# Kernel optimization log

Measured on AMD Instinct MI355X. Metric: run time of the kernel, lower is better.

## Reference

```python
import jax, jax.numpy as jnp
import numpy as np

B, H, TQ, TK, DH = 4, 8, 128, 128, 64
N_MEM, D_MEM, TOPK, HID = 100000, 512, 32, 128


def setup_inputs() -> dict:
    key = jax.random.key(0)
    ks = jax.random.split(key, 12)
    return {
        "q": jax.random.normal(ks[0], (B, H, TQ, DH), jnp.float32),
        "k_ctx": jax.random.normal(ks[1], (B, H, TK, DH), jnp.float32),
        "v_ctx": jax.random.normal(ks[2], (B, H, TK, DH), jnp.float32),
        "q_for_mem": jax.random.normal(ks[3], (B, TQ, D_MEM), jnp.float32),
        "mem_keys": jax.random.normal(ks[4], (N_MEM, D_MEM), jnp.float32),
        "mem_values": jax.random.normal(ks[5], (N_MEM, D_MEM), jnp.float32),
        "Wk": jax.random.normal(ks[6], (DH, D_MEM), jnp.float32) / np.sqrt(D_MEM),
        "Wv": jax.random.normal(ks[7], (DH, D_MEM), jnp.float32) / np.sqrt(D_MEM),
        "W1": jax.random.normal(ks[8], (HID, 2 * DH), jnp.float32) / np.sqrt(2 * DH),
        "b1": jnp.zeros((HID,), jnp.float32),
        "w2": jax.random.normal(ks[9], (HID,), jnp.float32) / np.sqrt(HID),
        "b2": jnp.zeros((1,), jnp.float32),
    }


def reference(q, k_ctx, v_ctx, q_for_mem, mem_keys, mem_values, Wk, Wv, W1, b1, w2, b2):
    # --- MemoryBank.retrieve: dense scores + top-k gather ---
    mem_scores = jnp.einsum('btd,nd->btn', q_for_mem, mem_keys)          # [B,TQ,N]
    _, idx = jax.lax.top_k(mem_scores, TOPK)                             # [B,TQ,K]
    K_mem = mem_keys[idx] @ Wk.T                                         # [B,TQ,K,DH] (mem_k_proj)
    V_mem = mem_values[idx] @ Wv.T                                       # [B,TQ,K,DH] (mem_v_proj)

    # --- ParametricScoreMLP: f([q;k]) = w2 . relu(W1q q + W1k k + b1) + b2 ---
    W1q, W1k = W1[:, :DH], W1[:, DH:]                                    # split concat linear
    q_part = jnp.einsum('bhtd,ed->bhte', q, W1q)                         # [B,H,TQ,HID]
    kctx_part = jnp.einsum('bhsd,ed->bhse', k_ctx, W1k)                  # [B,H,TK,HID]
    kmem_part = jnp.einsum('btkd,ed->btke', K_mem, W1k)                  # [B,TQ,K,HID]

    h_ctx = jax.nn.relu(q_part[:, :, :, None, :] + kctx_part[:, :, None, :, :] + b1)
    s_ctx = jnp.einsum('bhtse,e->bhts', h_ctx, w2) + b2[0]               # [B,H,TQ,TK]
    h_mem = jax.nn.relu(q_part[:, :, :, None, :] + kmem_part[:, None, :, :, :] + b1)
    s_mem = jnp.einsum('bhtke,e->bhtk', h_mem, w2) + b2[0]               # [B,H,TQ,K]

    scores = jnp.concatenate([s_ctx, s_mem], axis=-1)                    # [B,H,TQ,TK+K]
    weights = jax.nn.softmax(scores, axis=-1)

    w_ctx, w_mem = weights[..., :TK], weights[..., TK:]
    out = jnp.einsum('bhts,bhsd->bhtd', w_ctx, v_ctx) \
        + jnp.einsum('bhtk,btkd->bhtd', w_mem, V_mem)                    # [B,H,TQ,DH]
    return out, weights
```

## Files before the change

### kernel.cpp

```cpp
#include <hip/hip_runtime.h>
#include <cmath>

constexpr int B_ = 4, H_ = 8, TQ_ = 128, TK_ = 128, DH_ = 64;
constexpr int NMEM = 100000, DM = 512, TOPK = 32, HID = 128;
constexpr int R_ = B_ * TQ_;
constexpr int CTILE = 128, RTILE = 64;
constexpr int NCHP = 784;
constexpr int NPAD = NCHP * CTILE;
constexpr int KC = 16;
constexpr int NCAND = NCHP * KC;
constexpr int KSEL = 48;
constexpr int CAP  = 128;
constexpr int NLD  = NCAND / 256;

using f32x4  = __attribute__((ext_vector_type(4))) float;
using bf16x8 = __attribute__((ext_vector_type(8))) short;
using u16x8  = __attribute__((ext_vector_type(8))) unsigned short;

#define GLOAD16(g, l) __builtin_amdgcn_global_load_lds( \
    (const __attribute__((address_space(1))) void*)(g), \
    (__attribute__((address_space(3))) void*)(l), 16, 0, 0)

static __device__ __forceinline__ unsigned short f2bf(float f) {
    unsigned u = __float_as_uint(f);
    u = (u + 0x7FFFu + ((u >> 16) & 1u)) >> 16;
    return (unsigned short)u;
}

__global__ __launch_bounds__(256)
void k0_cvt(const float* __restrict__ src, unsigned short* __restrict__ dst,
            long n, long ntot)
{
    long stride = (long)gridDim.x * 256 * 8;
    for (long base = ((long)blockIdx.x * 256 + threadIdx.x) * 8; base < ntot; base += stride) {
        u16x8 o;
        if (base < n) {
            float4 v0 = *reinterpret_cast<const float4*>(src + base);
            float4 v1 = *reinterpret_cast<const float4*>(src + base + 4);
            o[0] = f2bf(v0.x); o[1] = f2bf(v0.y); o[2] = f2bf(v0.z); o[3] = f2bf(v0.w);
            o[4] = f2bf(v1.x); o[5] = f2bf(v1.y); o[6] = f2bf(v1.z); o[7] = f2bf(v1.w);
        } else {
            o = (u16x8)0;
        }
        *reinterpret_cast<u16x8*>(dst + base) = o;
    }
}

__global__ __launch_bounds__(256)
void k1_mfma(const unsigned short* __restrict__ qmb, const unsigned short* __restrict__ mkb,
             unsigned* __restrict__ cand_k, int* __restrict__ cand_i)
{
    const int wgid = blockIdx.x;
    const int xcd = wgid & 7;
    const int k9 = wgid >> 3;
    const int chunk = xcd * 98 + (k9 >> 3);
    const int rt = k9 & 7;
    const int row0 = rt * RTILE;
    const int col0 = chunk * CTILE;
    const int tid = threadIdx.x;
    const int lane = tid & 63, w = tid >> 6;
    const int wm = w >> 1, wn = w & 1;

    __shared__ __align__(16) char smem[64 * 132 * 4];
    char* Abase = smem;
    char* Bbase = smem + 8192;
    float* scf = (float*)smem;

    const char* srcA[2];
    const char* srcB[4];
#pragma unroll
    for (int p = 0; p < 2; ++p) {
        int X = p * 4096 + w * 1024 + lane * 16;
        int r = X >> 7, c = (X & 127) ^ ((r & 7) << 4);
        srcA[p] = (const char*)qmb + (size_t)(row0 + r) * 1024 + c;
    }
#pragma unroll
    for (int p = 0; p < 4; ++p) {
        int X = p * 4096 + w * 1024 + lane * 16;
        int r = X >> 7, c = (X & 127) ^ ((r & 7) << 4);
        srcB[p] = (const char*)mkb + (size_t)(col0 + r) * 1024 + c;
    }
    int aoff[2][2], boff[4][2];
#pragma unroll
    for (int mi = 0; mi < 2; ++mi) {
        int rr = wm * 32 + mi * 16 + (lane & 15);
        int bse = rr * 128 + ((lane >> 4) * 16);
        aoff[mi][0] = bse ^ ((rr & 7) << 4);
        aoff[mi][1] = (bse + 64) ^ ((rr & 7) << 4);
    }
#pragma unroll
    for (int ni = 0; ni < 4; ++ni) {
        int rr = wn * 64 + ni * 16 + (lane & 15);
        int bse = rr * 128 + ((lane >> 4) * 16);
        boff[ni][0] = 8192 + (bse ^ ((rr & 7) << 4));
        boff[ni][1] = 8192 + ((bse + 64) ^ ((rr & 7) << 4));
    }

    f32x4 acc[2][4];
#pragma unroll
    for (int mi = 0; mi < 2; ++mi)
#pragma unroll
        for (int ni = 0; ni < 4; ++ni) acc[mi][ni] = (f32x4)0.f;

    for (int ks = 0; ks < 8; ++ks) {
#pragma unroll
        for (int p = 0; p < 2; ++p) {
            GLOAD16(srcA[p], Abase + p * 4096 + w * 1024);
            srcA[p] += 128;
        }
#pragma unroll
        for (int p = 0; p < 4; ++p) {
            GLOAD16(srcB[p], Bbase + p * 4096 + w * 1024);
            srcB[p] += 128;
        }
        __syncthreads();
#pragma unroll
        for (int kk = 0; kk < 2; ++kk) {
            bf16x8 af[2], bfr[4];
#pragma unroll
            for (int mi = 0; mi < 2; ++mi)
                af[mi] = *reinterpret_cast<const bf16x8*>(smem + aoff[mi][kk]);
#pragma unroll
            for (int ni = 0; ni < 4; ++ni)
                bfr[ni] = *reinterpret_cast<const bf16x8*>(smem + boff[ni][kk]);
#pragma unroll
            for (int mi = 0; mi < 2; ++mi)
#pragma unroll
                for (int ni = 0; ni < 4; ++ni)
                    acc[mi][ni] = __builtin_amdgcn_mfma_f32_16x16x32_bf16(af[mi], bfr[ni], acc[mi][ni], 0, 0, 0);
        }
        __syncthreads();
    }

#pragma unroll
    for (int mi = 0; mi < 2; ++mi)
#pragma unroll
        for (int ni = 0; ni < 4; ++ni)
#pragma unroll
            for (int reg = 0; reg < 4; ++reg) {
                int rr = wm * 32 + mi * 16 + (lane >> 4) * 4 + reg;
                int cc = wn * 64 + ni * 16 + (lane & 15);
                scf[rr * 132 + cc] = (col0 + cc < NMEM) ? acc[mi][ni][reg] : -INFINITY;
            }
    __syncthreads();

    const int rid = tid >> 2, sub = tid & 3;
    const float* srow = scf + rid * 132;
    unsigned long long t0 = 0ull, t1 = 0ull, t2 = 0ull, t3 = 0ull;
#pragma unroll 8
    for (int i = 0; i < 32; ++i) {
        int c = sub + 4 * i;
        float v = srow[c];
        unsigned b = __float_as_uint(v);
        unsigned s = b ^ ((unsigned)((int)b >> 31) | 0x80000000u);
        unsigned long long k = ((unsigned long long)s << 7) | (unsigned)(127 - c);
        bool g0 = k > t0, g1 = k > t1, g2 = k > t2, g3 = k > t3;
        unsigned long long n0 = g0 ? k : t0;
        unsigned long long n1 = g0 ? t0 : (g1 ? k : t1);
        unsigned long long n2 = g1 ? t1 : (g2 ? k : t2);
        unsigned long long n3 = g2 ? t2 : (g3 ? k : t3);
        t0 = n0; t1 = n1; t2 = n2; t3 = n3;
    }
    size_t base = (size_t)(row0 + rid) * NCAND + (size_t)chunk * KC + sub * 4;
    uint4 kv, iv;
    kv.x = (unsigned)(t0 >> 7); iv.x = col0 + 127 - (int)(t0 & 127u);
    kv.y = (unsigned)(t1 >> 7); iv.y = col0 + 127 - (int)(t1 & 127u);
    kv.z = (unsigned)(t2 >> 7); iv.z = col0 + 127 - (int)(t2 & 127u);
    kv.w = (unsigned)(t3 >> 7); iv.w = col0 + 127 - (int)(t3 & 127u);
    *reinterpret_cast<uint4*>(cand_k + base) = kv;
    *reinterpret_cast<uint4*>(cand_i + base) = iv;
}

__global__ __launch_bounds__(256)
void k2a_thresh(const unsigned* __restrict__ cand_k, const int* __restrict__ cand_i,
                int* __restrict__ cand2_i, int* __restrict__ cand2_n)
{
    const int row = blockIdx.x;
    const int tid = threadIdx.x;
    const int lane = tid & 63, wv = tid >> 6;
    const unsigned* ck = cand_k + (size_t)row * NCAND;

    unsigned key[NLD];
#pragma unroll
    for (int j = 0; j < NLD; ++j) key[j] = ck[tid + j * 256];

    __shared__ int red[4];
    __shared__ int cnt;
    unsigned lo = 0u;
    int c_cur = NCAND;
    for (int bit = 31; bit >= 0; --bit) {
        if (c_cur <= CAP) break;
        unsigned T = lo | (1u << bit);
        int c = 0;
#pragma unroll
        for (int j = 0; j < NLD; ++j) c += (key[j] >= T);
#pragma unroll
        for (int off = 1; off < 64; off <<= 1) c += __shfl_xor(c, off);
        if (lane == 0) red[wv] = c;
        __syncthreads();
        int ct = red[0] + red[1] + red[2] + red[3];
        if (ct >= KSEL) { lo = T; c_cur = ct; }
        __syncthreads();
    }

    if (tid == 0) cnt = 0;
    __syncthreads();
#pragma unroll
    for (int j = 0; j < NLD; ++j) {
        if (key[j] >= lo) {
            int p = atomicAdd(&cnt, 1);
            if (p < CAP) cand2_i[(size_t)row * CAP + p] = cand_i[(size_t)row * NCAND + tid + j * 256];
        }
    }
    __syncthreads();
    if (tid == 0) cand2_n[row] = cnt < CAP ? cnt : CAP;
}

__global__ __launch_bounds__(256)
void k2b_rescore(const float* __restrict__ qm, const float* __restrict__ mk,
                 const int* __restrict__ cand2_i, const int* __restrict__ cand2_n,
                 double* __restrict__ rsc)
{
    const int row = blockIdx.x;
    const int tid = threadIdx.x;
    const int lane = tid & 63, wv = tid >> 6;
    const int c = blockIdx.y * 4 + wv;
    const int n = cand2_n[row];
    if (c >= n) return;
    const int idx = cand2_i[(size_t)row * CAP + c];
    const float* qrow = qm + (size_t)row * DM;
    const float* krow = mk + (size_t)idx * DM;
    double p = 0.0;
#pragma unroll
    for (int j = 0; j < DM / 64; ++j) {
        int d = lane + j * 64;
        p += (double)qrow[d] * (double)krow[d];
    }
#pragma unroll
    for (int off = 1; off < 64; off <<= 1) p += __shfl_xor(p, off);
    if (lane == 0) rsc[(size_t)row * CAP + c] = p;
}

__global__ __launch_bounds__(64)
void k2c_top32(const double* __restrict__ rsc, const int* __restrict__ cand2_i,
               const int* __restrict__ cand2_n, int* __restrict__ sel)
{
    const int row = blockIdx.x;
    const int lane = threadIdx.x;
    const int n = cand2_n[row];
    double v0 = -1.0e300, v1 = -1.0e300;
    int i0 = 0x7fffffff, i1 = 0x7fffffff;
    if (lane < n)      { v0 = rsc[(size_t)row * CAP + lane];      i0 = cand2_i[(size_t)row * CAP + lane]; }
    if (lane + 64 < n) { v1 = rsc[(size_t)row * CAP + lane + 64]; i1 = cand2_i[(size_t)row * CAP + lane + 64]; }
    for (int s = 0; s < TOPK; ++s) {
        double bv; int bi;
        if (v0 > v1 || (v0 == v1 && i0 < i1)) { bv = v0; bi = i0; }
        else                                  { bv = v1; bi = i1; }
#pragma unroll
        for (int off = 1; off < 64; off <<= 1) {
            double ov = __shfl_xor(bv, off);
            int    oi = __shfl_xor(bi, off);
            if (ov > bv || (ov == bv && oi < bi)) { bv = ov; bi = oi; }
        }
        if (lane == 0) sel[row * TOPK + s] = bi;
        if (i0 == bi) v0 = -1.0e300;
        if (i1 == bi) v1 = -1.0e300;
    }
}

__global__ __launch_bounds__(64)
void k3_proj(const float* __restrict__ mk, const float* __restrict__ mv,
             const float* __restrict__ Wk, const float* __restrict__ Wv,
             const int* __restrict__ sel,
             float* __restrict__ Kmem, float* __restrict__ Vmem)
{
    const int i0 = blockIdx.x * 8;
    const int tid = threadIdx.x;
    __shared__ float s[2][8][DM];
    __shared__ int si[8];
    if (tid < 8) si[tid] = sel[i0 + tid];
    __syncthreads();
    for (int l = tid; l < 1024; l += 64) {
        int r = l >> 7, c4 = l & 127;
        *reinterpret_cast<float4*>(&s[0][r][c4 * 4]) =
            *reinterpret_cast<const float4*>(mk + (size_t)si[r] * DM + c4 * 4);
        *reinterpret_cast<float4*>(&s[1][r][c4 * 4]) =
            *reinterpret_cast<const float4*>(mv + (size_t)si[r] * DM + c4 * 4);
    }
    __syncthreads();
    const int doV = tid >> 5;
    const int ep = tid & 31;
    const float* W = doV ? Wv : Wk;
    const float* w0 = W + (size_t)ep * DM;
    const float* w1 = W + (size_t)(ep + 32) * DM;
    float a0[8], a1[8];
#pragma unroll
    for (int r = 0; r < 8; ++r) { a0[r] = 0.f; a1[r] = 0.f; }
    for (int d4 = 0; d4 < DM / 4; ++d4) {
        float4 x0 = *reinterpret_cast<const float4*>(w0 + d4 * 4);
        float4 x1 = *reinterpret_cast<const float4*>(w1 + d4 * 4);
#pragma unroll
        for (int r = 0; r < 8; ++r) {
            float4 m = *reinterpret_cast<const float4*>(&s[doV][r][d4 * 4]);
            a0[r] = fmaf(x0.x, m.x, fmaf(x0.y, m.y, fmaf(x0.z, m.z, fmaf(x0.w, m.w, a0[r]))));
            a1[r] = fmaf(x1.x, m.x, fmaf(x1.y, m.y, fmaf(x1.z, m.z, fmaf(x1.w, m.w, a1[r]))));
        }
    }
    float* O = doV ? Vmem : Kmem;
#pragma unroll
    for (int r = 0; r < 8; ++r) {
        O[(size_t)(i0 + r) * DH_ + ep] = a0[r];
        O[(size_t)(i0 + r) * DH_ + ep + 32] = a1[r];
    }
}

__global__ __launch_bounds__(128)
void k4_parts(const float* __restrict__ q, const float* __restrict__ kctx,
              const float* __restrict__ Kmem, const float* __restrict__ W1,
              float* __restrict__ qp, float* __restrict__ kcp, float* __restrict__ kmp)
{
    const int bid = blockIdx.x;
    const int tid = threadIdx.x;
    const float* src; float* dst; int woff;
    if (bid < 1024)      { int r0 = bid * 4;          src = q    + (size_t)r0 * DH_; dst = qp  + (size_t)r0 * HID; woff = 0; }
    else if (bid < 2048) { int r0 = (bid - 1024) * 4; src = kctx + (size_t)r0 * DH_; dst = kcp + (size_t)r0 * HID; woff = DH_; }
    else                 { int r0 = (bid - 2048) * 4; src = Kmem + (size_t)r0 * DH_; dst = kmp + (size_t)r0 * HID; woff = DH_; }
    __shared__ float s[4][DH_];
    for (int l = tid; l < 4 * DH_; l += 128) s[l >> 6][l & 63] = src[l];
    __syncthreads();
    const float* wr = W1 + (size_t)tid * (2 * DH_) + woff;
    float a0 = 0.f, a1 = 0.f, a2 = 0.f, a3 = 0.f;
#pragma unroll 8
    for (int d = 0; d < DH_; ++d) {
        float w = wr[d];
        a0 = fmaf(s[0][d], w, a0);
        a1 = fmaf(s[1][d], w, a1);
        a2 = fmaf(s[2][d], w, a2);
        a3 = fmaf(s[3][d], w, a3);
    }
    dst[0 * HID + tid] = a0;
    dst[1 * HID + tid] = a1;
    dst[2 * HID + tid] = a2;
    dst[3 * HID + tid] = a3;
}

__global__ __launch_bounds__(256)
void k5_attn(const float* __restrict__ qp, const float* __restrict__ kcp,
             const float* __restrict__ kmp, const float* __restrict__ vctx,
             const float* __restrict__ Vmem, const float* __restrict__ b1,
             const float* __restrict__ w2, const float* __restrict__ b2,
             float* __restrict__ out, float* __restrict__ outw)
{
    const int bid = blockIdx.x;
    const int t = bid & 127, h = (bid >> 7) & 7, b = bid >> 10;
    const int tid = threadIdx.x;
    const int lane = tid & 63, wv = tid >> 6;
    const int bh = b * H_ + h, bht = bh * TQ_ + t, bt = b * TQ_ + t;
    constexpr int NS = TK_ + TOPK;
    __shared__ float qps[HID], b1s[HID], w2s[HID];
    __shared__ float sc[NS];
    __shared__ float red[8];
    if (tid < HID) {
        qps[tid] = qp[(size_t)bht * HID + tid];
        b1s[tid] = b1[tid];
        w2s[tid] = w2[tid];
    }
    __syncthreads();
    const float bias2 = b2[0];
    if (tid < NS) {
        const float* kr = (tid < TK_) ? (kcp + ((size_t)bh * TK_ + tid) * HID)
                                      : (kmp + ((size_t)bt * TOPK + (tid - TK_)) * HID);
        float acc = 0.f;
#pragma unroll 4
        for (int e4 = 0; e4 < HID / 4; ++e4) {
            float4 kv = *reinterpret_cast<const float4*>(kr + e4 * 4);
            acc += fmaxf(qps[e4 * 4 + 0] + kv.x + b1s[e4 * 4 + 0], 0.f) * w2s[e4 * 4 + 0];
            acc += fmaxf(qps[e4 * 4 + 1] + kv.y + b1s[e4 * 4 + 1], 0.f) * w2s[e4 * 4 + 1];
            acc += fmaxf(qps[e4 * 4 + 2] + kv.z + b1s[e4 * 4 + 2], 0.f) * w2s[e4 * 4 + 2];
            acc += fmaxf(qps[e4 * 4 + 3] + kv.w + b1s[e4 * 4 + 3], 0.f) * w2s[e4 * 4 + 3];
        }
        sc[tid] = acc + bias2;
    }
    __syncthreads();
    float v = (tid < NS) ? sc[tid] : -INFINITY;
    float m = v;
#pragma unroll
    for (int off = 1; off < 64; off <<= 1) m = fmaxf(m, __shfl_xor(m, off));
    if (lane == 0) red[wv] = m;
    __syncthreads();
    if (tid == 0) red[4] = fmaxf(fmaxf(red[0], red[1]), fmaxf(red[2], red[3]));
    __syncthreads();
    const float mm = red[4];
    float e = (tid < NS) ? expf(v - mm) : 0.f;
    float ssum = e;
#pragma unroll
    for (int off = 1; off < 64; off <<= 1) ssum += __shfl_xor(ssum, off);
    if (lane == 0) red[wv] = ssum;
    __syncthreads();
    if (tid == 0) red[5] = red[0] + red[1] + red[2] + red[3];
    __syncthreads();
    const float inv = 1.f / red[5];
    if (tid < NS) {
        float w = e * inv;
        sc[tid] = w;
        outw[(size_t)bht * NS + tid] = w;
    }
    __syncthreads();
    if (tid < DH_) {
        float acc = 0.f;
        const float* vb = vctx + (size_t)bh * TK_ * DH_ + tid;
        for (int s2 = 0; s2 < TK_; ++s2) acc = fmaf(sc[s2], vb[(size_t)s2 * DH_], acc);
        const float* vm = Vmem + (size_t)bt * TOPK * DH_ + tid;
#pragma unroll
        for (int kk = 0; kk < TOPK; ++kk) acc = fmaf(sc[TK_ + kk], vm[(size_t)kk * DH_], acc);
        out[(size_t)bht * DH_ + tid] = acc;
    }
}

extern "C" void kernel_launch(void* const* d_in, const int* in_sizes, int n_in,
                              void* d_out, int out_size, void* d_ws, size_t ws_size,
                              hipStream_t stream)
{
    const float* q    = (const float*)d_in[0];
    const float* kctx = (const float*)d_in[1];
    const float* vctx = (const float*)d_in[2];
    const float* qm   = (const float*)d_in[3];
    const float* mk   = (const float*)d_in[4];
    const float* mv   = (const float*)d_in[5];
    const float* Wk   = (const float*)d_in[6];
    const float* Wv   = (const float*)d_in[7];
    const float* W1   = (const float*)d_in[8];
    const float* b1   = (const float*)d_in[9];
    const float* w2   = (const float*)d_in[10];
    const float* b2   = (const float*)d_in[11];
    float* out  = (float*)d_out;
    float* outw = out + (size_t)B_ * H_ * TQ_ * DH_;

    char* w = (char*)d_ws;
    unsigned short* mkb = (unsigned short*)w; w += sizeof(unsigned short) * (size_t)NPAD * DM;
    unsigned short* qmb = (unsigned short*)w; w += sizeof(unsigned short) * R_ * DM;
    unsigned* cand_k = (unsigned*)w; w += sizeof(unsigned) * (size_t)R_ * NCAND;
    int*   cand_i = (int*)w;   w += sizeof(int) * (size_t)R_ * NCAND;
    int*   cand2_i= (int*)w;   w += sizeof(int) * R_ * CAP;
    int*   cand2_n= (int*)w;   w += sizeof(int) * R_;
    double* rsc   = (double*)w; w += sizeof(double) * R_ * CAP;
    int*   sel    = (int*)w;   w += sizeof(int) * R_ * TOPK;
    float* Kmem   = (float*)w; w += sizeof(float) * R_ * TOPK * DH_;
    float* Vmem   = (float*)w; w += sizeof(float) * R_ * TOPK * DH_;
    float* qp     = (float*)w; w += sizeof(float) * B_ * H_ * TQ_ * HID;
    float* kcp    = (float*)w; w += sizeof(float) * B_ * H_ * TK_ * HID;
    float* kmp    = (float*)w; w += sizeof(float) * R_ * TOPK * HID;

    hipLaunchKernelGGL(k0_cvt, dim3(2048), dim3(256), 0, stream,
                       mk, mkb, (long)NMEM * DM, (long)NPAD * DM);
    hipLaunchKernelGGL(k0_cvt, dim3(128), dim3(256), 0, stream,
                       qm, qmb, (long)R_ * DM, (long)R_ * DM);
    hipLaunchKernelGGL(k1_mfma, dim3(NCHP * 8), dim3(256), 0, stream, qmb, mkb, cand_k, cand_i);
    hipLaunchKernelGGL(k2a_thresh, dim3(R_), dim3(256), 0, stream, cand_k, cand_i, cand2_i, cand2_n);
    hipLaunchKernelGGL(k2b_rescore, dim3(R_, CAP / 4), dim3(256), 0, stream, qm, mk, cand2_i, cand2_n, rsc);
    hipLaunchKernelGGL(k2c_top32, dim3(R_), dim3(64), 0, stream, rsc, cand2_i, cand2_n, sel);
    hipLaunchKernelGGL(k3_proj, dim3(R_ * TOPK / 8), dim3(64), 0, stream, mk, mv, Wk, Wv, sel, Kmem, Vmem);
    hipLaunchKernelGGL(k4_parts, dim3(6144), dim3(128), 0, stream, q, kctx, Kmem, W1, qp, kcp, kmp);
    hipLaunchKernelGGL(k5_attn, dim3(B_ * H_ * TQ_), dim3(256), 0, stream, qp, kcp, kmp, vctx, Vmem, b1, w2, b2, out, outw);
}
```

Baseline: 361.0 us.

## Merge bf16 conversions, vectorize chunk top-4, widen projection and attention PV

The two bf16 conversion launches become one, relying on qmb sitting right after mkb in the workspace. In k1 the score tile is stored transposed so each thread reads contiguous float4s, and its top-4 selection uses 32-bit keys that reuse the low 7 mantissa bits for the column index instead of 64-bit keys. The rescore loop reads float4 vectors, k3_proj runs 128 threads with one output column each, and the k5 P·V product is split across all four waves with a shared-memory reduction. Truncating the key's mantissa bits coarsens candidate ordering, but the later fp64 rescore over a wider candidate set should absorb this.

```diff
diff --git a/kernel.cpp b/kernel.cpp
--- a/kernel.cpp
+++ b/kernel.cpp
@@ -28,15 +28,23 @@
 }
 
 __global__ __launch_bounds__(256)
-void k0_cvt(const float* __restrict__ src, unsigned short* __restrict__ dst,
-            long n, long ntot)
-{
+void k0_cvt(const float* __restrict__ mk, const float* __restrict__ qm,
+            unsigned short* __restrict__ dst)
+{
+    const long totalmk = (long)NPAD * DM;
+    const long nvalid  = (long)NMEM * DM;
+    const long total   = totalmk + (long)R_ * DM;
     long stride = (long)gridDim.x * 256 * 8;
-    for (long base = ((long)blockIdx.x * 256 + threadIdx.x) * 8; base < ntot; base += stride) {
+    for (long base = ((long)blockIdx.x * 256 + threadIdx.x) * 8; base < total; base += stride) {
         u16x8 o;
-        if (base < n) {
-            float4 v0 = *reinterpret_cast<const float4*>(src + base);
-            float4 v1 = *reinterpret_cast<const float4*>(src + base + 4);
+        const float* src = nullptr;
+        long off = 0;
+        if (base < totalmk) {
+            if (base < nvalid) { src = mk; off = base; }
+        } else { src = qm; off = base - totalmk; }
+        if (src) {
+            float4 v0 = *reinterpret_cast<const float4*>(src + off);
+            float4 v1 = *reinterpret_cast<const float4*>(src + off + 4);
             o[0] = f2bf(v0.x); o[1] = f2bf(v0.y); o[2] = f2bf(v0.z); o[3] = f2bf(v0.w);
             o[4] = f2bf(v1.x); o[5] = f2bf(v1.y); o[6] = f2bf(v1.z); o[7] = f2bf(v1.w);
         } else {
@@ -140,33 +148,38 @@
             for (int reg = 0; reg < 4; ++reg) {
                 int rr = wm * 32 + mi * 16 + (lane >> 4) * 4 + reg;
                 int cc = wn * 64 + ni * 16 + (lane & 15);
-                scf[rr * 132 + cc] = (col0 + cc < NMEM) ? acc[mi][ni][reg] : -INFINITY;
+                int pos = ((cc & 31) << 2) | (cc >> 5);
+                scf[rr * 132 + pos] = (col0 + cc < NMEM) ? acc[mi][ni][reg] : -INFINITY;
             }
     __syncthreads();
 
     const int rid = tid >> 2, sub = tid & 3;
-    const float* srow = scf + rid * 132;
-    unsigned long long t0 = 0ull, t1 = 0ull, t2 = 0ull, t3 = 0ull;
-#pragma unroll 8
-    for (int i = 0; i < 32; ++i) {
-        int c = sub + 4 * i;
-        float v = srow[c];
-        unsigned b = __float_as_uint(v);
-        unsigned s = b ^ ((unsigned)((int)b >> 31) | 0x80000000u);
-        unsigned long long k = ((unsigned long long)s << 7) | (unsigned)(127 - c);
-        bool g0 = k > t0, g1 = k > t1, g2 = k > t2, g3 = k > t3;
-        unsigned long long n0 = g0 ? k : t0;
-        unsigned long long n1 = g0 ? t0 : (g1 ? k : t1);
-        unsigned long long n2 = g1 ? t1 : (g2 ? k : t2);
-        unsigned long long n3 = g2 ? t2 : (g3 ? k : t3);
-        t0 = n0; t1 = n1; t2 = n2; t3 = n3;
+    const float* srow = scf + rid * 132 + sub * 32;
+    const int bsub = 127 - sub * 8;
+    unsigned t0 = 0u, t1 = 0u, t2 = 0u, t3 = 0u;
+#pragma unroll
+    for (int i = 0; i < 8; ++i) {
+        float4 v4 = *reinterpret_cast<const float4*>(srow + i * 4);
+        float vv[4] = {v4.x, v4.y, v4.z, v4.w};
+#pragma unroll
+        for (int q = 0; q < 4; ++q) {
+            unsigned b = __float_as_uint(vv[q]);
+            unsigned s = b ^ ((unsigned)((int)b >> 31) | 0x80000000u);
+            unsigned key = (s & 0xFFFFFF80u) | (unsigned)(bsub - (q * 32 + i));
+            bool g0 = key > t0, g1 = key > t1, g2 = key > t2, g3 = key > t3;
+            unsigned n0 = g0 ? key : t0;
+            unsigned n1 = g0 ? t0 : (g1 ? key : t1);
+            unsigned n2 = g1 ? t1 : (g2 ? key : t2);
+            unsigned n3 = g2 ? t2 : (g3 ? key : t3);
+            t0 = n0; t1 = n1; t2 = n2; t3 = n3;
+        }
     }
     size_t base = (size_t)(row0 + rid) * NCAND + (size_t)chunk * KC + sub * 4;
     uint4 kv, iv;
-    kv.x = (unsigned)(t0 >> 7); iv.x = col0 + 127 - (int)(t0 & 127u);
-    kv.y = (unsigned)(t1 >> 7); iv.y = col0 + 127 - (int)(t1 & 127u);
-    kv.z = (unsigned)(t2 >> 7); iv.z = col0 + 127 - (int)(t2 & 127u);
-    kv.w = (unsigned)(t3 >> 7); iv.w = col0 + 127 - (int)(t3 & 127u);
+    kv.x = t0; iv.x = col0 + 127 - (int)(t0 & 127u);
+    kv.y = t1; iv.y = col0 + 127 - (int)(t1 & 127u);
+    kv.z = t2; iv.z = col0 + 127 - (int)(t2 & 127u);
+    kv.w = t3; iv.w = col0 + 127 - (int)(t3 & 127u);
     *reinterpret_cast<uint4*>(cand_k + base) = kv;
     *reinterpret_cast<uint4*>(cand_i + base) = iv;
 }
@@ -228,14 +241,14 @@
     const int n = cand2_n[row];
     if (c >= n) return;
     const int idx = cand2_i[(size_t)row * CAP + c];
-    const float* qrow = qm + (size_t)row * DM;
-    const float* krow = mk + (size_t)idx * DM;
-    double p = 0.0;
-#pragma unroll
-    for (int j = 0; j < DM / 64; ++j) {
-        int d = lane + j * 64;
-        p += (double)qrow[d] * (double)krow[d];
-    }
+    const float4* q4 = reinterpret_cast<const float4*>(qm + (size_t)row * DM);
+    const float4* k4 = reinterpret_cast<const float4*>(mk + (size_t)idx * DM);
+    float4 a0 = q4[lane], b0 = k4[lane];
+    float4 a1 = q4[lane + 64], b1 = k4[lane + 64];
+    double p = (double)a0.x * b0.x + (double)a0.y * b0.y
+             + (double)a0.z * b0.z + (double)a0.w * b0.w
+             + (double)a1.x * b1.x + (double)a1.y * b1.y
+             + (double)a1.z * b1.z + (double)a1.w * b1.w;
 #pragma unroll
     for (int off = 1; off < 64; off <<= 1) p += __shfl_xor(p, off);
     if (lane == 0) rsc[(size_t)row * CAP + c] = p;
@@ -268,7 +281,7 @@
     }
 }
 
-__global__ __launch_bounds__(64)
+__global__ __launch_bounds__(128)
 void k3_proj(const float* __restrict__ mk, const float* __restrict__ mv,
              const float* __restrict__ Wk, const float* __restrict__ Wv,
              const int* __restrict__ sel,
@@ -280,38 +293,31 @@
     __shared__ int si[8];
     if (tid < 8) si[tid] = sel[i0 + tid];
     __syncthreads();
-    for (int l = tid; l < 1024; l += 64) {
-        int r = l >> 7, c4 = l & 127;
-        *reinterpret_cast<float4*>(&s[0][r][c4 * 4]) =
-            *reinterpret_cast<const float4*>(mk + (size_t)si[r] * DM + c4 * 4);
-        *reinterpret_cast<float4*>(&s[1][r][c4 * 4]) =
-            *reinterpret_cast<const float4*>(mv + (size_t)si[r] * DM + c4 * 4);
-    }
-    __syncthreads();
-    const int doV = tid >> 5;
-    const int ep = tid & 31;
-    const float* W = doV ? Wv : Wk;
-    const float* w0 = W + (size_t)ep * DM;
-    const float* w1 = W + (size_t)(ep + 32) * DM;
-    float a0[8], a1[8];
-#pragma unroll
-    for (int r = 0; r < 8; ++r) { a0[r] = 0.f; a1[r] = 0.f; }
+    for (int l = tid; l < 2048; l += 128) {
+        int mat = l >> 10, r = (l >> 7) & 7, c4 = l & 127;
+        const float* src = (mat ? mv : mk) + (size_t)si[r] * DM + c4 * 4;
+        *reinterpret_cast<float4*>(&s[mat][r][c4 * 4]) =
+            *reinterpret_cast<const float4*>(src);
+    }
+    __syncthreads();
+    const int doV = tid >> 6;
+    const int ep = tid & 63;
+    const float* w0 = (doV ? Wv : Wk) + (size_t)ep * DM;
+    float a0[8];
+#pragma unroll
+    for (int r = 0; r < 8; ++r) a0[r] = 0.f;
     for (int d4 = 0; d4 < DM / 4; ++d4) {
         float4 x0 = *reinterpret_cast<const float4*>(w0 + d4 * 4);
-        float4 x1 = *reinterpret_cast<const float4*>(w1 + d4 * 4);
 #pragma unroll
         for (int r = 0; r < 8; ++r) {
             float4 m = *reinterpret_cast<const float4*>(&s[doV][r][d4 * 4]);
             a0[r] = fmaf(x0.x, m.x, fmaf(x0.y, m.y, fmaf(x0.z, m.z, fmaf(x0.w, m.w, a0[r]))));
-            a1[r] = fmaf(x1.x, m.x, fmaf(x1.y, m.y, fmaf(x1.z, m.z, fmaf(x1.w, m.w, a1[r]))));
         }
     }
     float* O = doV ? Vmem : Kmem;
 #pragma unroll
-    for (int r = 0; r < 8; ++r) {
+    for (int r = 0; r < 8; ++r)
         O[(size_t)(i0 + r) * DH_ + ep] = a0[r];
-        O[(size_t)(i0 + r) * DH_ + ep + 32] = a1[r];
-    }
 }
 
 __global__ __launch_bounds__(128)
@@ -360,6 +366,7 @@
     __shared__ float qps[HID], b1s[HID], w2s[HID];
     __shared__ float sc[NS];
     __shared__ float red[8];
+    __shared__ float part[4][DH_];
     if (tid < HID) {
         qps[tid] = qp[(size_t)bht * HID + tid];
         b1s[tid] = b1[tid];
@@ -406,15 +413,21 @@
         outw[(size_t)bht * NS + tid] = w;
     }
     __syncthreads();
-    if (tid < DH_) {
+    {
+        const int d = lane;
+        const int s0 = wv * 40;
         float acc = 0.f;
-        const float* vb = vctx + (size_t)bh * TK_ * DH_ + tid;
-        for (int s2 = 0; s2 < TK_; ++s2) acc = fmaf(sc[s2], vb[(size_t)s2 * DH_], acc);
-        const float* vm = Vmem + (size_t)bt * TOPK * DH_ + tid;
-#pragma unroll
-        for (int kk = 0; kk < TOPK; ++kk) acc = fmaf(sc[TK_ + kk], vm[(size_t)kk * DH_], acc);
-        out[(size_t)bht * DH_ + tid] = acc;
-    }
+        for (int s2 = s0; s2 < s0 + 40; ++s2) {
+            const float* vrow = (s2 < TK_)
+                ? (vctx + ((size_t)bh * TK_ + s2) * DH_)
+                : (Vmem + ((size_t)bt * TOPK + (s2 - TK_)) * DH_);
+            acc = fmaf(sc[s2], vrow[d], acc);
+        }
+        part[wv][d] = acc;
+    }
+    __syncthreads();
+    if (tid < DH_)
+        out[(size_t)bht * DH_ + tid] = part[0][tid] + part[1][tid] + part[2][tid] + part[3][tid];
 }
 
 extern "C" void kernel_launch(void* const* d_in, const int* in_sizes, int n_in,
@@ -451,15 +464,12 @@
     float* kcp    = (float*)w; w += sizeof(float) * B_ * H_ * TK_ * HID;
     float* kmp    = (float*)w; w += sizeof(float) * R_ * TOPK * HID;
 
-    hipLaunchKernelGGL(k0_cvt, dim3(2048), dim3(256), 0, stream,
-                       mk, mkb, (long)NMEM * DM, (long)NPAD * DM);
-    hipLaunchKernelGGL(k0_cvt, dim3(128), dim3(256), 0, stream,
-                       qm, qmb, (long)R_ * DM, (long)R_ * DM);
+    hipLaunchKernelGGL(k0_cvt, dim3(4096), dim3(256), 0, stream, mk, qm, mkb);
     hipLaunchKernelGGL(k1_mfma, dim3(NCHP * 8), dim3(256), 0, stream, qmb, mkb, cand_k, cand_i);
     hipLaunchKernelGGL(k2a_thresh, dim3(R_), dim3(256), 0, stream, cand_k, cand_i, cand2_i, cand2_n);
     hipLaunchKernelGGL(k2b_rescore, dim3(R_, CAP / 4), dim3(256), 0, stream, qm, mk, cand2_i, cand2_n, rsc);
     hipLaunchKernelGGL(k2c_top32, dim3(R_), dim3(64), 0, stream, rsc, cand2_i, cand2_n, sel);
-    hipLaunchKernelGGL(k3_proj, dim3(R_ * TOPK / 8), dim3(64), 0, stream, mk, mv, Wk, Wv, sel, Kmem, Vmem);
+    hipLaunchKernelGGL(k3_proj, dim3(R_ * TOPK / 8), dim3(128), 0, stream, mk, mv, Wk, Wv, sel, Kmem, Vmem);
     hipLaunchKernelGGL(k4_parts, dim3(6144), dim3(128), 0, stream, q, kctx, Kmem, W1, qp, kcp, kmp);
     hipLaunchKernelGGL(k5_attn, dim3(B_ * H_ * TQ_), dim3(256), 0, stream, qp, kcp, kmp, vctx, Vmem, b1, w2, b2, out, outw);
 }
```

Result: no change. 364.1 us (+0.9%).
